# Kernel tuning notes

Hardware: AMD Instinct MI355X
Metric: run time of the kernel (lower is better)

The kernel has to match this reference:

```python
import jax, jax.numpy as jnp
import numpy as np
from jax import lax

B, L, D_MODEL = 2, 2048, 768
D_STATE, D_INNER, DT_RANK, K = 16, 1536, 48, 4


def setup_inputs() -> dict:
    key = jax.random.key(0)
    ks = jax.random.split(key, 10)
    x = jax.random.normal(ks[0], (B, L, D_MODEL), dtype=jnp.float32)
    in_proj_w = 0.02 * jax.random.normal(ks[1], (2 * D_INNER, D_MODEL), dtype=jnp.float32)
    conv_w = 0.1 * jax.random.normal(ks[2], (D_INNER, 1, K), dtype=jnp.float32)
    conv_b = 0.01 * jax.random.normal(ks[3], (D_INNER,), dtype=jnp.float32)
    # A_log initialized as log(1..d_state) per channel (as in _init_parameters)
    A_log = jnp.tile(jnp.log(jnp.arange(1, D_STATE + 1, dtype=jnp.float32)), (D_INNER, 1))
    D_param = jnp.ones((D_INNER,), dtype=jnp.float32)
    x_proj_w = 0.02 * jax.random.normal(ks[4], (DT_RANK + 2 * D_STATE, D_INNER), dtype=jnp.float32)
    dt_proj_w = jax.random.uniform(ks[5], (D_INNER, DT_RANK), minval=-0.1, maxval=0.1, dtype=jnp.float32)
    dt_proj_b = 0.01 * jax.random.normal(ks[6], (D_INNER,), dtype=jnp.float32)
    out_proj_w = 0.02 * jax.random.normal(ks[7], (D_MODEL, D_INNER), dtype=jnp.float32)
    return {"x": x, "in_proj_w": in_proj_w, "conv_w": conv_w, "conv_b": conv_b,
            "A_log": A_log, "D_param": D_param, "x_proj_w": x_proj_w,
            "dt_proj_w": dt_proj_w, "dt_proj_b": dt_proj_b, "out_proj_w": out_proj_w}


def _forward(x, in_proj_w, conv_w, conv_b, A_log, D_param, x_proj_w, dt_proj_w, dt_proj_b, out_proj_w):
    xz = jnp.einsum('bld,ed->ble', x, in_proj_w)            # [B,L,2*d_inner]
    xp, z = jnp.split(xz, 2, axis=-1)                        # [B,L,d_inner] each
    # depthwise causal conv1d: torch Conv1d(padding=3)[..., :L] == left-pad 3, valid conv
    xc = lax.conv_general_dilated(
        xp.transpose(0, 2, 1), conv_w, window_strides=(1,),
        padding=[(K - 1, 0)], feature_group_count=D_INNER)   # [B,d_inner,L]
    xc = (xc + conv_b[None, :, None]).transpose(0, 2, 1)     # [B,L,d_inner]
    xc = jax.nn.silu(xc)
    x_dbl = jnp.einsum('bld,ed->ble', xc, x_proj_w)          # [B,L,dt_rank+2*d_state]
    dt_low, Bmat, Cmat = jnp.split(x_dbl, [DT_RANK, DT_RANK + D_STATE], axis=-1)
    dt = jax.nn.softplus(jnp.einsum('blr,dr->bld', dt_low, dt_proj_w) + dt_proj_b)  # [B,L,d_inner]
    A = -jnp.exp(A_log)                                      # [d_inner,d_state]
    A_bar = jnp.exp(dt[..., None] * A[None, None])           # [B,L,d_inner,d_state]
    Bx = (dt * xc)[..., None] * Bmat[:, :, None, :]          # [B,L,d_inner,d_state]
    # time-major scan over the recurrence h = A_bar*h + B_bar*x
    A_t = A_bar.transpose(1, 0, 2, 3)
    Bx_t = Bx.transpose(1, 0, 2, 3)
    C_t = Cmat.transpose(1, 0, 2)                            # [L,B,d_state]
    h0 = jnp.zeros((B, D_INNER, D_STATE), dtype=x.dtype)

    def step(h, inp):
        a, bx, c = inp
        h = a * h + bx
        y = jnp.einsum('bds,bs->bd', h, c)
        return h, y

    _, ys = lax.scan(step, h0, (A_t, Bx_t, C_t))             # ys: [L,B,d_inner]
    y = ys.transpose(1, 0, 2)
    y = y + xc * D_param
    y = y * jax.nn.silu(z)
    return jnp.einsum('bld,md->blm', y, out_proj_w)          # [B,L,d_model]


def reference(x, in_proj_w, conv_w, conv_b, A_log, D_param, x_proj_w, dt_proj_w, dt_proj_b, out_proj_w):
    return _forward(x, in_proj_w, conv_w, conv_b, A_log, D_param, x_proj_w, dt_proj_w, dt_proj_b, out_proj_w)
```

## Files before the change

kernel.cpp:

```cpp
#include <hip/hip_runtime.h>
#include <stdint.h>

#define B_SZ    2
#define L_SEQ   2048
#define DMODEL  768
#define DSTATE  16
#define DINNER  1536
#define DTRANK  48
#define M_ROWS  4096
#define NSEG    8
#define SEGL    256
#define NSC     8
#define SCL     32
#define KSPLIT  8

typedef __attribute__((ext_vector_type(8))) short bf16x8;
typedef __attribute__((ext_vector_type(4))) float f32x4;
typedef __attribute__((ext_vector_type(2))) float f32x2;
typedef __attribute__((ext_vector_type(4))) unsigned int u32x4;
typedef __attribute__((ext_vector_type(2))) unsigned int u32x2;

__device__ __forceinline__ unsigned short f2bf(float f) {
  unsigned int u = __float_as_uint(f);
  u += 0x7FFFu + ((u >> 16) & 1u);
  return (unsigned short)(u >> 16);
}
__device__ __forceinline__ unsigned int pack2bf(float a, float b) {
  return (unsigned int)f2bf(a) | ((unsigned int)f2bf(b) << 16);
}
__device__ __forceinline__ float bf2f(unsigned short h) {
  return __uint_as_float(((unsigned int)h) << 16);
}
__device__ __forceinline__ float fexp(float x) {
  return __builtin_amdgcn_exp2f(x * 1.44269504088896340736f);
}
__device__ __forceinline__ float sigm(float x) {
  return 1.0f / (1.0f + fexp(-x));
}

template <int CTRL>
__device__ __forceinline__ float dpp_add(float v) {
  int x = __builtin_amdgcn_update_dpp(0, __float_as_int(v), CTRL, 0xF, 0xF, true);
  return v + __int_as_float(x);
}
__device__ __forceinline__ float quad_sum(float v) {
  v = dpp_add<0xB1>(v);
  v = dpp_add<0x4E>(v);
  return v;
}
__device__ __forceinline__ float row16_sum(float v) {
  v = dpp_add<0xB1>(v);
  v = dpp_add<0x4E>(v);
  v = dpp_add<0x124>(v);
  v = dpp_add<0x128>(v);
  return v;
}

__global__ void cast_all_kernel(const float* __restrict__ x, const float* __restrict__ w1,
                                const float* __restrict__ w2, const float* __restrict__ w3,
                                const float* __restrict__ dtw,
                                unsigned short* __restrict__ xbf, unsigned short* __restrict__ w1bf,
                                unsigned short* __restrict__ w2bf, unsigned short* __restrict__ w3bf,
                                unsigned short* __restrict__ dtwbf) {
  int i = blockIdx.x * 256 + threadIdx.x;
  const int n_x = M_ROWS * DMODEL;
  const int n_w1 = 2 * DINNER * DMODEL;
  const int n_w3 = DMODEL * DINNER;
  const int n_w2 = 128 * DINNER;
  const int n_dtw = DINNER * 64;
  if (i < n_x)  { xbf[i] = f2bf(x[i]); return; }  i -= n_x;
  if (i < n_w1) { w1bf[i] = f2bf(w1[i]); return; } i -= n_w1;
  if (i < n_w3) { w3bf[i] = f2bf(w3[i]); return; } i -= n_w3;
  if (i < n_w2) {
    int row = i / DINNER, col = i - row * DINNER;
    w2bf[i] = (row < (DTRANK + 2 * DSTATE)) ? f2bf(w2[row * DINNER + col]) : (unsigned short)0;
    return;
  }
  i -= n_w2;
  if (i < n_dtw) {
    int row = i >> 6, col = i & 63;
    dtwbf[i] = (col < DTRANK) ? f2bf(dtw[row * DTRANK + col]) : (unsigned short)0;
  }
}

__global__ void xdbl_pack_kernel(const float* __restrict__ xdblS,
                                 unsigned short* __restrict__ dtlbf,
                                 float* __restrict__ BCt) {
  const int SLAB = M_ROWS * 128;
  int i = blockIdx.x * 256 + threadIdx.x;
  const int n_dtl = M_ROWS * 64;
  if (i < n_dtl) {
    int row = i >> 6, col = i & 63;
    if (col < DTRANK) {
      float v = 0.f;
#pragma unroll
      for (int z = 0; z < KSPLIT; z++) v += xdblS[(size_t)z * SLAB + row * 128 + col];
      dtlbf[i] = f2bf(v);
    } else dtlbf[i] = 0;
    return;
  }
  i -= n_dtl;
  int l4 = i & 511;
  int j  = (i >> 9) & 31;
  int b  = (i >> 14) & 1;
  f32x4 o;
#pragma unroll
  for (int k = 0; k < 4; k++) {
    float v = 0.f;
    size_t base = ((size_t)b * L_SEQ + l4 * 4 + k) * 128 + DTRANK + j;
#pragma unroll
    for (int z = 0; z < KSPLIT; z++) v += xdblS[(size_t)z * SLAB + base];
    o[k] = v;
  }
  *(f32x4*)(BCt + ((size_t)b * 32 + j) * L_SEQ + l4 * 4) = o;
}

template <int EPI>
__global__ __launch_bounds__(256, 2) void gemm_bt(
    const unsigned short* __restrict__ A, const unsigned short* __restrict__ Bt,
    float* __restrict__ C, int K, int KS, int ldc, long slab,
    const float* __restrict__ bias) {
  __shared__ unsigned short As[128 * 40];
  __shared__ unsigned short Bs[128 * 40];
  const int tid = threadIdx.x;
  const int m0 = blockIdx.x * 128;
  const int n0 = blockIdx.y * 128;
  const int ks = blockIdx.z * KS, ke = ks + KS;
  float* Cz = C + (size_t)blockIdx.z * slab;
  const int lane = tid & 63;
  const int wave = tid >> 6;
  const int wr = (wave >> 1) * 64, wc = (wave & 1) * 64;
  const int lm = lane & 15, q = lane >> 4;
  const int r = tid >> 2, sg = (tid & 3) * 8;

  f32x4 acc[4][4] = {};

  for (int k0 = ks; k0 < ke; k0 += 32) {
    u32x4 a0 = *(const u32x4*)(A + (size_t)(m0 + r) * K + k0 + sg);
    u32x4 a1 = *(const u32x4*)(A + (size_t)(m0 + r + 64) * K + k0 + sg);
    u32x4 b0 = *(const u32x4*)(Bt + (size_t)(n0 + r) * K + k0 + sg);
    u32x4 b1 = *(const u32x4*)(Bt + (size_t)(n0 + r + 64) * K + k0 + sg);
    __syncthreads();
    *(u32x4*)&As[r * 40 + sg] = a0;
    *(u32x4*)&As[(r + 64) * 40 + sg] = a1;
    *(u32x4*)&Bs[r * 40 + sg] = b0;
    *(u32x4*)&Bs[(r + 64) * 40 + sg] = b1;
    __syncthreads();
    bf16x8 af[4], bq[4];
#pragma unroll
    for (int mt = 0; mt < 4; mt++)
      af[mt] = *(const bf16x8*)&As[(wr + mt * 16 + lm) * 40 + q * 8];
#pragma unroll
    for (int nt = 0; nt < 4; nt++)
      bq[nt] = *(const bf16x8*)&Bs[(wc + nt * 16 + lm) * 40 + q * 8];
#pragma unroll
    for (int mt = 0; mt < 4; mt++)
#pragma unroll
      for (int nt = 0; nt < 4; nt++)
        acc[mt][nt] = __builtin_amdgcn_mfma_f32_16x16x32_bf16(af[mt], bq[nt], acc[mt][nt], 0, 0, 0);
  }

#pragma unroll
  for (int mt = 0; mt < 4; mt++) {
    int row0 = m0 + wr + mt * 16 + q * 4;
    float bs4[4];
    if (EPI == 2) {
#pragma unroll
      for (int i = 0; i < 4; i++) bs4[i] = bias[row0 + i];
    }
#pragma unroll
    for (int nt = 0; nt < 4; nt++) {
      int col = n0 + wc + nt * 16 + lm;
#pragma unroll
      for (int i = 0; i < 4; i++) {
        float v = acc[mt][nt][i];
        if (EPI == 2) {
          v += bs4[i];
          v = (v > 15.f) ? v : log1pf(fexp(v));
        }
        Cz[(size_t)(row0 + i) * ldc + col] = v;
      }
    }
  }
}

__global__ __launch_bounds__(256) void conv_silu_t(const float* __restrict__ xz,
                                                   const float* __restrict__ cw,
                                                   const float* __restrict__ cb,
                                                   unsigned short* __restrict__ xcbf,
                                                   unsigned short* __restrict__ xcT) {
  __shared__ float tl[67 * 68];
  __shared__ unsigned short xs[64 * 80];
  __shared__ float cws[64 * 4];
  __shared__ float cbs[64];
  const int r0 = blockIdx.x * 64;
  const int c0 = blockIdx.y * 64;
  const int t = threadIdx.x;
  cws[t] = cw[(c0 + (t >> 2)) * 4 + (t & 3)];
  if (t < 64) cbs[t] = cb[c0 + t];
  const bool lowedge = (r0 & (L_SEQ - 1)) == 0;
#pragma unroll
  for (int it = 0; it < 5; it++) {
    int idx = t + it * 256;
    int rr = idx >> 4;
    int cs4 = (idx & 15) * 4;
    if (rr < 67) {
      f32x4 v;
      if (lowedge && rr < 3) v = (f32x4){0.f, 0.f, 0.f, 0.f};
      else v = *(const f32x4*)(xz + (size_t)(r0 + rr - 3) * 3072 + c0 + cs4);
      *(f32x4*)&tl[rr * 68 + cs4] = v;
    }
  }
  __syncthreads();
  const int cs = (t & 15) * 4;
  f32x4 w0, w1, w2, w3, cbv;
#pragma unroll
  for (int j = 0; j < 4; j++) {
    w0[j] = cws[(cs + j) * 4 + 0];
    w1[j] = cws[(cs + j) * 4 + 1];
    w2[j] = cws[(cs + j) * 4 + 2];
    w3[j] = cws[(cs + j) * 4 + 3];
    cbv[j] = cbs[cs + j];
  }
#pragma unroll
  for (int it = 0; it < 4; it++) {
    int r = (t >> 4) + it * 16;
    f32x4 t0 = *(const f32x4*)&tl[(r + 0) * 68 + cs];
    f32x4 t1 = *(const f32x4*)&tl[(r + 1) * 68 + cs];
    f32x4 t2 = *(const f32x4*)&tl[(r + 2) * 68 + cs];
    f32x4 t3 = *(const f32x4*)&tl[(r + 3) * 68 + cs];
    f32x4 acc = cbv + w0 * t0 + w1 * t1 + w2 * t2 + w3 * t3;
#pragma unroll
    for (int j = 0; j < 4; j++) acc[j] = acc[j] * sigm(acc[j]);
    u32x2 pk;
    pk[0] = pack2bf(acc[0], acc[1]);
    pk[1] = pack2bf(acc[2], acc[3]);
    *(u32x2*)(xcbf + (size_t)(r0 + r) * DINNER + c0 + cs) = pk;
    *(u32x2*)&xs[r * 80 + cs] = pk;
  }
  __syncthreads();
#pragma unroll
  for (int it = 0; it < 2; it++) {
    int idx = t + it * 256;
    int cc = idx & 63, rs = idx >> 6;
    unsigned int w[4];
#pragma unroll
    for (int p = 0; p < 4; p++) {
      unsigned int lo = xs[(rs * 8 + 2 * p) * 80 + cc];
      unsigned int hi = xs[(rs * 8 + 2 * p + 1) * 80 + cc];
      w[p] = lo | (hi << 16);
    }
    *(u32x4*)(xcT + (size_t)(c0 + cc) * M_ROWS + r0 + rs * 8) = *(u32x4*)w;
  }
}

__global__ __launch_bounds__(256) void transpose_silu(const float* __restrict__ xz,
                                                      unsigned short* __restrict__ out) {
  __shared__ float tl[64 * 68];
  const int r0 = blockIdx.x * 64;
  const int c0 = blockIdx.y * 64;
  const int tid = threadIdx.x;
#pragma unroll
  for (int it = 0; it < 4; it++) {
    int idx = tid + it * 256;
    int rr = idx >> 4, cs = idx & 15;
    f32x4 v = *(const f32x4*)(xz + (size_t)(r0 + rr) * 3072 + DINNER + c0 + cs * 4);
#pragma unroll
    for (int p = 0; p < 4; p++) v[p] = v[p] * sigm(v[p]);
    *(f32x4*)&tl[rr * 68 + cs * 4] = v;
  }
  __syncthreads();
#pragma unroll
  for (int it = 0; it < 2; it++) {
    int idx = tid + it * 256;
    int cc = idx & 63, rs = idx >> 6;
    unsigned int w[4];
#pragma unroll
    for (int p = 0; p < 4; p++)
      w[p] = pack2bf(tl[(rs * 8 + 2 * p) * 68 + cc], tl[(rs * 8 + 2 * p + 1) * 68 + cc]);
    *(u32x4*)(out + (size_t)(c0 + cc) * M_ROWS + r0 + rs * 8) = *(u32x4*)w;
  }
}

struct SC32 { f32x2 dt; unsigned int xc, sz; f32x4 B0, B1, C0, C1; };

template <int FULL>
__global__ __launch_bounds__(64) void scan_seg(
    const float* __restrict__ dtT, const unsigned short* __restrict__ xcT,
    const float* __restrict__ BCt, const unsigned short* __restrict__ szT,
    const float* __restrict__ A_log, const float* __restrict__ Dp,
    const float* __restrict__ HIN, float* __restrict__ P, float* __restrict__ HL,
    unsigned short* __restrict__ ybf) {
  __shared__ float dtS[4 * 36];
  __shared__ float dtxS[4 * 36];
  __shared__ float BS[16 * 36];
  __shared__ float CS[FULL ? 16 * 36 : 1];
  __shared__ unsigned int xcR[FULL ? 4 * 18 : 1];
  __shared__ unsigned int szR[FULL ? 4 * 18 : 1];
  __shared__ float ysh[FULL ? 16 * 36 : 1];
  const int lane = threadIdx.x;
  const int s = lane & 15, dl = lane >> 4;
  const int d0 = blockIdx.x * 4;
  const int d = d0 + dl;
  const int b = blockIdx.y;
  const int seg = blockIdx.z;
  const int lseg = seg * SEGL;
  const size_t rbase = (size_t)b * L_SEQ + lseg;
  const float a2 = -fexp(A_log[d * 16 + s]) * 1.44269504f;
  const float dpv = Dp[d];
  const float* dtbase = dtT + (size_t)d0 * M_ROWS + rbase;
  const unsigned short* xcbase = xcT + (size_t)d0 * M_ROWS + rbase;
  const unsigned short* szbase = szT + (size_t)d0 * M_ROWS + rbase;
  const float* Bbase = BCt + (size_t)b * 32 * L_SEQ + lseg;
  const float* Cbase = Bbase + 16 * L_SEQ;
  const int ch = lane >> 4, li = lane & 15;
  const int s4 = lane >> 2, lj = lane & 3;
  float* ywp = &ysh[(dl * 4 + (s >> 2)) * 36 + (s & 3)];
  const bool sb0 = (s & 1) != 0, sb1 = (s & 2) != 0;
  float h = 0.f, sdt = 0.f;
  size_t o = (((size_t)seg * B_SZ + b) * DINNER + d) * 16 + s;
  if (FULL) h = HIN[o];

  auto load32 = [&](SC32& R, int l0) {
    R.dt = *(const f32x2*)(dtbase + (size_t)ch * M_ROWS + l0 + li * 2);
    R.xc = *(const unsigned int*)(xcbase + (size_t)ch * M_ROWS + l0 + li * 2);
    if (FULL) R.sz = *(const unsigned int*)(szbase + (size_t)ch * M_ROWS + l0 + li * 2);
    R.B0 = *(const f32x4*)(Bbase + (size_t)s4 * L_SEQ + l0 + lj * 8);
    R.B1 = *(const f32x4*)(Bbase + (size_t)s4 * L_SEQ + l0 + lj * 8 + 4);
    if (FULL) {
      R.C0 = *(const f32x4*)(Cbase + (size_t)s4 * L_SEQ + l0 + lj * 8);
      R.C1 = *(const f32x4*)(Cbase + (size_t)s4 * L_SEQ + l0 + lj * 8 + 4);
    }
  };
  auto store32 = [&](const SC32& R) {
    if (!FULL) sdt += R.dt[0] + R.dt[1];
    f32x2 xf, dtx;
    xf[0] = __uint_as_float(R.xc << 16);
    xf[1] = __uint_as_float(R.xc & 0xFFFF0000u);
    dtx = R.dt * xf;
    *(f32x2*)&dtS[ch * 36 + li * 2] = R.dt;
    *(f32x2*)&dtxS[ch * 36 + li * 2] = dtx;
    if (FULL) {
      xcR[ch * 18 + li] = R.xc;
      szR[ch * 18 + li] = R.sz;
    }
    *(f32x4*)&BS[s4 * 36 + lj * 8] = R.B0;
    *(f32x4*)&BS[s4 * 36 + lj * 8 + 4] = R.B1;
    if (FULL) {
      *(f32x4*)&CS[s4 * 36 + lj * 8] = R.C0;
      *(f32x4*)&CS[s4 * 36 + lj * 8 + 4] = R.C1;
    }
  };

#pragma unroll 1
  for (int c = 0; c < NSC; c++) {
    SC32 R;
    load32(R, c * SCL);
    store32(R);
#pragma unroll
    for (int g = 0; g < 4; g++) {
      const int l0g = g * 8;
      f32x4 dta = *(const f32x4*)&dtS[dl * 36 + l0g];
      f32x4 dtb = *(const f32x4*)&dtS[dl * 36 + l0g + 4];
      f32x4 xa  = *(const f32x4*)&dtxS[dl * 36 + l0g];
      f32x4 xb  = *(const f32x4*)&dtxS[dl * 36 + l0g + 4];
      f32x4 Ba  = *(const f32x4*)&BS[s * 36 + l0g];
      f32x4 Bb  = *(const f32x4*)&BS[s * 36 + l0g + 4];
      f32x4 Ca, Cb;
      if (FULL) {
        Ca = *(const f32x4*)&CS[s * 36 + l0g];
        Cb = *(const f32x4*)&CS[s * 36 + l0g + 4];
      }
      float p8[8];
#pragma unroll
      for (int j = 0; j < 8; j++) {
        float dtj = (j < 4) ? dta[j] : dtb[j - 4];
        float dxj = (j < 4) ? xa[j]  : xb[j - 4];
        float Bj  = (j < 4) ? Ba[j]  : Bb[j - 4];
        float a = __builtin_amdgcn_exp2f(dtj * a2);
        h = a * h + dxj * Bj;
        if (FULL) {
          float Cj = (j < 4) ? Ca[j] : Cb[j - 4];
          p8[j] = h * Cj;
        }
      }
      if (FULL) {
#pragma unroll
        for (int half = 0; half < 2; half++) {
          float q0 = quad_sum(p8[half * 4 + 0]);
          float q1 = quad_sum(p8[half * 4 + 1]);
          float q2 = quad_sum(p8[half * 4 + 2]);
          float q3 = quad_sum(p8[half * 4 + 3]);
          float v01 = sb0 ? q1 : q0;
          float v23 = sb0 ? q3 : q2;
          ywp[g * 8 + half * 4] = sb1 ? v23 : v01;
        }
      }
    }
    if (FULL) {
      f32x2 y0 = *(const f32x2*)&ysh[(dl * 4 + 0) * 36 + s * 2];
      f32x2 y1 = *(const f32x2*)&ysh[(dl * 4 + 1) * 36 + s * 2];
      f32x2 y2 = *(const f32x2*)&ysh[(dl * 4 + 2) * 36 + s * 2];
      f32x2 y3 = *(const f32x2*)&ysh[(dl * 4 + 3) * 36 + s * 2];
      f32x2 ys = y0 + y1 + y2 + y3;
      unsigned int xcu = xcR[dl * 18 + s];
      unsigned int szu = szR[dl * 18 + s];
      float xcf[2] = {__uint_as_float(xcu << 16), __uint_as_float(xcu & 0xFFFF0000u)};
      float szf[2] = {__uint_as_float(szu << 16), __uint_as_float(szu & 0xFFFF0000u)};
      size_t rr0 = rbase + c * SCL + s * 2;
#pragma unroll
      for (int i = 0; i < 2; i++) {
        float yv = ys[i] + xcf[i] * dpv;
        ybf[(rr0 + i) * DINNER + d] = f2bf(yv * szf[i]);
      }
    }
  }
  if (!FULL) {
    sdt = row16_sum(sdt);
    P[o] = __builtin_amdgcn_exp2f(a2 * sdt);
    HL[o] = h;
  }
}

__global__ void scan_comb(const float* __restrict__ P, const float* __restrict__ HL,
                          float* __restrict__ HIN) {
  int tg = blockIdx.x * 256 + threadIdx.x;
  int s = tg & 15;
  int rem = tg >> 4;
  int d = rem % DINNER;
  int b = rem / DINNER;
  float h = 0.f;
  for (int g = 0; g < NSEG; g++) {
    size_t o = (((size_t)g * B_SZ + b) * DINNER + d) * 16 + s;
    HIN[o] = h;
    if (g < NSEG - 1) h = P[o] * h + HL[o];
  }
}

extern "C" void kernel_launch(void* const* d_in, const int* in_sizes, int n_in,
                              void* d_out, int out_size, void* d_ws, size_t ws_size,
                              hipStream_t stream) {
  const float* x    = (const float*)d_in[0];
  const float* w1   = (const float*)d_in[1];
  const float* cw   = (const float*)d_in[2];
  const float* cb   = (const float*)d_in[3];
  const float* alog = (const float*)d_in[4];
  const float* Dp   = (const float*)d_in[5];
  const float* w2   = (const float*)d_in[6];
  const float* dtw  = (const float*)d_in[7];
  const float* dtb  = (const float*)d_in[8];
  const float* w3   = (const float*)d_in[9];
  float* out = (float*)d_out;
  char* ws = (char*)d_ws;

  size_t off = 0;
  auto alloc = [&](size_t bytes) { size_t o = off; off += (bytes + 255) & ~(size_t)255; return o; };
  char*           xzr   = ws + alloc((size_t)M_ROWS * 3072 * 4);
  float*          xz    = (float*)xzr;
  float*          dtT   = (float*)xzr;
  unsigned short* ybf   = (unsigned short*)(xzr + (size_t)DINNER * M_ROWS * 4);
  float*          xdblS = (float*)(ws + alloc((size_t)KSPLIT * M_ROWS * 128 * 4));
  unsigned short* xbf   = (unsigned short*)(ws + alloc((size_t)M_ROWS * DMODEL * 2));
  unsigned short* w1bf  = (unsigned short*)(ws + alloc((size_t)2 * DINNER * DMODEL * 2));
  unsigned short* w2bf  = (unsigned short*)(ws + alloc((size_t)128 * DINNER * 2));
  unsigned short* w3bf  = (unsigned short*)(ws + alloc((size_t)DMODEL * DINNER * 2));
  unsigned short* dtlbf = (unsigned short*)(ws + alloc((size_t)M_ROWS * 64 * 2));
  unsigned short* dtwbf = (unsigned short*)(ws + alloc((size_t)DINNER * 64 * 2));
  unsigned short* xcbf  = (unsigned short*)(ws + alloc((size_t)M_ROWS * DINNER * 2));
  unsigned short* xcT   = (unsigned short*)(ws + alloc((size_t)DINNER * M_ROWS * 2));
  unsigned short* szbf  = (unsigned short*)(ws + alloc((size_t)DINNER * M_ROWS * 2));
  float*          BCt   = (float*)(ws + alloc((size_t)B_SZ * 32 * L_SEQ * 4));
  float*          Pbuf  = (float*)(ws + alloc((size_t)NSEG * B_SZ * DINNER * 16 * 4));
  float*          HLbuf = (float*)(ws + alloc((size_t)NSEG * B_SZ * DINNER * 16 * 4));
  float*          HINb  = (float*)(ws + alloc((size_t)NSEG * B_SZ * DINNER * 16 * 4));

  cast_all_kernel<<<27264, 256, 0, stream>>>(x, w1, w2, w3, dtw, xbf, w1bf, w2bf, w3bf, dtwbf);
  gemm_bt<0><<<dim3(32, 24), 256, 0, stream>>>(xbf, w1bf, xz, DMODEL, DMODEL, 3072, 0, nullptr);
  conv_silu_t<<<dim3(64, 24), 256, 0, stream>>>(xz, cw, cb, xcbf, xcT);
  transpose_silu<<<dim3(64, 24), 256, 0, stream>>>(xz, szbf);
  gemm_bt<0><<<dim3(32, 1, KSPLIT), 256, 0, stream>>>(xcbf, w2bf, xdblS, DINNER,
                                                      DINNER / KSPLIT, 128,
                                                      (long)M_ROWS * 128, nullptr);
  xdbl_pack_kernel<<<1152, 256, 0, stream>>>(xdblS, dtlbf, BCt);
  gemm_bt<2><<<dim3(12, 32), 256, 0, stream>>>(dtwbf, dtlbf, dtT, 64, 64, M_ROWS, 0, dtb);
  scan_seg<0><<<dim3(384, 2, NSEG - 1), 64, 0, stream>>>(dtT, xcT, BCt, szbf, alog, Dp,
                                                         nullptr, Pbuf, HLbuf, nullptr);
  scan_comb<<<192, 256, 0, stream>>>(Pbuf, HLbuf, HINb);
  scan_seg<1><<<dim3(384, 2, NSEG), 64, 0, stream>>>(dtT, xcT, BCt, szbf, alog, Dp,
                                                     HINb, nullptr, nullptr, ybf);
  gemm_bt<0><<<dim3(32, 6), 256, 0, stream>>>(ybf, w3bf, out, DINNER, DINNER, 768, 0, nullptr);
}
```

Measured before the change: 304.6 us.

## Use direct global-to-LDS loads in GEMMs, fuse z-transpose into conv, widen scan blocks

The three plain GEMMs now use a new kernel that moves tiles straight from global memory into LDS through global_load_lds. This drops the register staging step, but the LDS tile loses its padding, which risks bank conflicts. The separate silu(z) transpose kernel is merged into the conv kernel to save one launch and reuse the tile buffer. The scan kernels now pack four independent waves into each 256-thread block instead of one wave per block.

```diff
diff --git a/kernel.cpp b/kernel.cpp
--- a/kernel.cpp
+++ b/kernel.cpp
@@ -28,9 +28,6 @@
 __device__ __forceinline__ unsigned int pack2bf(float a, float b) {
   return (unsigned int)f2bf(a) | ((unsigned int)f2bf(b) << 16);
 }
-__device__ __forceinline__ float bf2f(unsigned short h) {
-  return __uint_as_float(((unsigned int)h) << 16);
-}
 __device__ __forceinline__ float fexp(float x) {
   return __builtin_amdgcn_exp2f(x * 1.44269504088896340736f);
 }
@@ -54,6 +51,11 @@
   v = dpp_add<0x124>(v);
   v = dpp_add<0x128>(v);
   return v;
+}
+
+__device__ __forceinline__ void gload_lds(const unsigned short* g, unsigned short* l) {
+  __builtin_amdgcn_global_load_lds((__attribute__((address_space(1))) void*)g,
+                                   (__attribute__((address_space(3))) void*)l, 16, 0, 0);
 }
 
 __global__ void cast_all_kernel(const float* __restrict__ x, const float* __restrict__ w1,
@@ -115,18 +117,68 @@
   *(f32x4*)(BCt + ((size_t)b * 32 + j) * L_SEQ + l4 * 4) = o;
 }
 
-template <int EPI>
-__global__ __launch_bounds__(256, 2) void gemm_bt(
+__global__ __launch_bounds__(256, 2) void gemm_async(
     const unsigned short* __restrict__ A, const unsigned short* __restrict__ Bt,
-    float* __restrict__ C, int K, int KS, int ldc, long slab,
-    const float* __restrict__ bias) {
+    float* __restrict__ C, int K, int KS, int ldc, long slab) {
+  __shared__ unsigned short As[128 * 32];
+  __shared__ unsigned short Bs[128 * 32];
+  const int tid = threadIdx.x;
+  const int lane = tid & 63;
+  const int wv = tid >> 6;
+  const int m0 = blockIdx.x * 128;
+  const int n0 = blockIdx.y * 128;
+  const int ks = blockIdx.z * KS, ke = ks + KS;
+  float* Cz = C + (size_t)blockIdx.z * slab;
+  const int wr = (wv >> 1) * 64, wc = (wv & 1) * 64;
+  const int lm = lane & 15, q = lane >> 4;
+  const int srow = wv * 16 + (lane >> 2);
+  const int scol = (lane & 3) * 8;
+
+  f32x4 acc[4][4] = {};
+
+  for (int k0 = ks; k0 < ke; k0 += 32) {
+#pragma unroll
+    for (int j = 0; j < 2; j++) {
+      gload_lds(A + (size_t)(m0 + j * 64 + srow) * K + k0 + scol, &As[(j * 64 + wv * 16) * 32]);
+      gload_lds(Bt + (size_t)(n0 + j * 64 + srow) * K + k0 + scol, &Bs[(j * 64 + wv * 16) * 32]);
+    }
+    __syncthreads();
+    bf16x8 af[4], bq[4];
+#pragma unroll
+    for (int mt = 0; mt < 4; mt++)
+      af[mt] = *(const bf16x8*)&As[(wr + mt * 16 + lm) * 32 + q * 8];
+#pragma unroll
+    for (int nt = 0; nt < 4; nt++)
+      bq[nt] = *(const bf16x8*)&Bs[(wc + nt * 16 + lm) * 32 + q * 8];
+#pragma unroll
+    for (int mt = 0; mt < 4; mt++)
+#pragma unroll
+      for (int nt = 0; nt < 4; nt++)
+        acc[mt][nt] = __builtin_amdgcn_mfma_f32_16x16x32_bf16(af[mt], bq[nt], acc[mt][nt], 0, 0, 0);
+    __syncthreads();
+  }
+
+#pragma unroll
+  for (int mt = 0; mt < 4; mt++) {
+    int row0 = m0 + wr + mt * 16 + q * 4;
+#pragma unroll
+    for (int nt = 0; nt < 4; nt++) {
+      int col = n0 + wc + nt * 16 + lm;
+#pragma unroll
+      for (int i = 0; i < 4; i++)
+        Cz[(size_t)(row0 + i) * ldc + col] = acc[mt][nt][i];
+    }
+  }
+}
+
+__global__ __launch_bounds__(256, 2) void gemm_dt(
+    const unsigned short* __restrict__ A, const unsigned short* __restrict__ Bt,
+    float* __restrict__ C, int K, int ldc, const float* __restrict__ bias) {
   __shared__ unsigned short As[128 * 40];
   __shared__ unsigned short Bs[128 * 40];
   const int tid = threadIdx.x;
   const int m0 = blockIdx.x * 128;
   const int n0 = blockIdx.y * 128;
-  const int ks = blockIdx.z * KS, ke = ks + KS;
-  float* Cz = C + (size_t)blockIdx.z * slab;
   const int lane = tid & 63;
   const int wave = tid >> 6;
   const int wr = (wave >> 1) * 64, wc = (wave & 1) * 64;
@@ -135,7 +187,7 @@
 
   f32x4 acc[4][4] = {};
 
-  for (int k0 = ks; k0 < ke; k0 += 32) {
+  for (int k0 = 0; k0 < K; k0 += 32) {
     u32x4 a0 = *(const u32x4*)(A + (size_t)(m0 + r) * K + k0 + sg);
     u32x4 a1 = *(const u32x4*)(A + (size_t)(m0 + r + 64) * K + k0 + sg);
     u32x4 b0 = *(const u32x4*)(Bt + (size_t)(n0 + r) * K + k0 + sg);
@@ -164,34 +216,30 @@
   for (int mt = 0; mt < 4; mt++) {
     int row0 = m0 + wr + mt * 16 + q * 4;
     float bs4[4];
-    if (EPI == 2) {
-#pragma unroll
-      for (int i = 0; i < 4; i++) bs4[i] = bias[row0 + i];
-    }
+#pragma unroll
+    for (int i = 0; i < 4; i++) bs4[i] = bias[row0 + i];
 #pragma unroll
     for (int nt = 0; nt < 4; nt++) {
       int col = n0 + wc + nt * 16 + lm;
 #pragma unroll
       for (int i = 0; i < 4; i++) {
-        float v = acc[mt][nt][i];
-        if (EPI == 2) {
-          v += bs4[i];
-          v = (v > 15.f) ? v : log1pf(fexp(v));
-        }
-        Cz[(size_t)(row0 + i) * ldc + col] = v;
+        float v = acc[mt][nt][i] + bs4[i];
+        v = (v > 15.f) ? v : log1pf(fexp(v));
+        C[(size_t)(row0 + i) * ldc + col] = v;
       }
     }
   }
 }
 
-__global__ __launch_bounds__(256) void conv_silu_t(const float* __restrict__ xz,
-                                                   const float* __restrict__ cw,
-                                                   const float* __restrict__ cb,
-                                                   unsigned short* __restrict__ xcbf,
-                                                   unsigned short* __restrict__ xcT) {
+__global__ __launch_bounds__(256) void conv_silu_zt(const float* __restrict__ xz,
+                                                    const float* __restrict__ cw,
+                                                    const float* __restrict__ cb,
+                                                    unsigned short* __restrict__ xcbf,
+                                                    unsigned short* __restrict__ xcT,
+                                                    unsigned short* __restrict__ szT) {
   __shared__ float tl[67 * 68];
   __shared__ unsigned short xs[64 * 80];
-  __shared__ float cws[64 * 4];
+  __shared__ float cws[256];
   __shared__ float cbs[64];
   const int r0 = blockIdx.x * 64;
   const int c0 = blockIdx.y * 64;
@@ -212,33 +260,44 @@
     }
   }
   __syncthreads();
-  const int cs = (t & 15) * 4;
-  f32x4 w0, w1, w2, w3, cbv;
-#pragma unroll
-  for (int j = 0; j < 4; j++) {
-    w0[j] = cws[(cs + j) * 4 + 0];
-    w1[j] = cws[(cs + j) * 4 + 1];
-    w2[j] = cws[(cs + j) * 4 + 2];
-    w3[j] = cws[(cs + j) * 4 + 3];
-    cbv[j] = cbs[cs + j];
-  }
+  {
+    const int cs = (t & 15) * 4;
+    f32x4 w0, w1, w2, w3, cbv;
+#pragma unroll
+    for (int j = 0; j < 4; j++) {
+      w0[j] = cws[(cs + j) * 4 + 0];
+      w1[j] = cws[(cs + j) * 4 + 1];
+      w2[j] = cws[(cs + j) * 4 + 2];
+      w3[j] = cws[(cs + j) * 4 + 3];
+      cbv[j] = cbs[cs + j];
+    }
+#pragma unroll
+    for (int it = 0; it < 4; it++) {
+      int r = (t >> 4) + it * 16;
+      f32x4 t0 = *(const f32x4*)&tl[(r + 0) * 68 + cs];
+      f32x4 t1 = *(const f32x4*)&tl[(r + 1) * 68 + cs];
+      f32x4 t2 = *(const f32x4*)&tl[(r + 2) * 68 + cs];
+      f32x4 t3 = *(const f32x4*)&tl[(r + 3) * 68 + cs];
+      f32x4 acc = cbv + w0 * t0 + w1 * t1 + w2 * t2 + w3 * t3;
+#pragma unroll
+      for (int j = 0; j < 4; j++) acc[j] = acc[j] * sigm(acc[j]);
+      u32x2 pk;
+      pk[0] = pack2bf(acc[0], acc[1]);
+      pk[1] = pack2bf(acc[2], acc[3]);
+      *(u32x2*)(xcbf + (size_t)(r0 + r) * DINNER + c0 + cs) = pk;
+      *(u32x2*)&xs[r * 80 + cs] = pk;
+    }
+  }
+  __syncthreads();
 #pragma unroll
   for (int it = 0; it < 4; it++) {
-    int r = (t >> 4) + it * 16;
-    f32x4 t0 = *(const f32x4*)&tl[(r + 0) * 68 + cs];
-    f32x4 t1 = *(const f32x4*)&tl[(r + 1) * 68 + cs];
-    f32x4 t2 = *(const f32x4*)&tl[(r + 2) * 68 + cs];
-    f32x4 t3 = *(const f32x4*)&tl[(r + 3) * 68 + cs];
-    f32x4 acc = cbv + w0 * t0 + w1 * t1 + w2 * t2 + w3 * t3;
-#pragma unroll
-    for (int j = 0; j < 4; j++) acc[j] = acc[j] * sigm(acc[j]);
-    u32x2 pk;
-    pk[0] = pack2bf(acc[0], acc[1]);
-    pk[1] = pack2bf(acc[2], acc[3]);
-    *(u32x2*)(xcbf + (size_t)(r0 + r) * DINNER + c0 + cs) = pk;
-    *(u32x2*)&xs[r * 80 + cs] = pk;
-  }
-  __syncthreads();
+    int idx = t + it * 256;
+    int rr = idx >> 4, cs = idx & 15;
+    f32x4 v = *(const f32x4*)(xz + (size_t)(r0 + rr) * 3072 + DINNER + c0 + cs * 4);
+#pragma unroll
+    for (int p = 0; p < 4; p++) v[p] = v[p] * sigm(v[p]);
+    *(f32x4*)&tl[rr * 68 + cs * 4] = v;
+  }
 #pragma unroll
   for (int it = 0; it < 2; it++) {
     int idx = t + it * 256;
@@ -252,55 +311,40 @@
     }
     *(u32x4*)(xcT + (size_t)(c0 + cc) * M_ROWS + r0 + rs * 8) = *(u32x4*)w;
   }
-}
-
-__global__ __launch_bounds__(256) void transpose_silu(const float* __restrict__ xz,
-                                                      unsigned short* __restrict__ out) {
-  __shared__ float tl[64 * 68];
-  const int r0 = blockIdx.x * 64;
-  const int c0 = blockIdx.y * 64;
-  const int tid = threadIdx.x;
-#pragma unroll
-  for (int it = 0; it < 4; it++) {
-    int idx = tid + it * 256;
-    int rr = idx >> 4, cs = idx & 15;
-    f32x4 v = *(const f32x4*)(xz + (size_t)(r0 + rr) * 3072 + DINNER + c0 + cs * 4);
-#pragma unroll
-    for (int p = 0; p < 4; p++) v[p] = v[p] * sigm(v[p]);
-    *(f32x4*)&tl[rr * 68 + cs * 4] = v;
-  }
   __syncthreads();
 #pragma unroll
   for (int it = 0; it < 2; it++) {
-    int idx = tid + it * 256;
+    int idx = t + it * 256;
     int cc = idx & 63, rs = idx >> 6;
     unsigned int w[4];
 #pragma unroll
     for (int p = 0; p < 4; p++)
       w[p] = pack2bf(tl[(rs * 8 + 2 * p) * 68 + cc], tl[(rs * 8 + 2 * p + 1) * 68 + cc]);
-    *(u32x4*)(out + (size_t)(c0 + cc) * M_ROWS + r0 + rs * 8) = *(u32x4*)w;
+    *(u32x4*)(szT + (size_t)(c0 + cc) * M_ROWS + r0 + rs * 8) = *(u32x4*)w;
   }
 }
 
 struct SC32 { f32x2 dt; unsigned int xc, sz; f32x4 B0, B1, C0, C1; };
 
 template <int FULL>
-__global__ __launch_bounds__(64) void scan_seg(
+__global__ __launch_bounds__(256) void scan_seg(
     const float* __restrict__ dtT, const unsigned short* __restrict__ xcT,
     const float* __restrict__ BCt, const unsigned short* __restrict__ szT,
     const float* __restrict__ A_log, const float* __restrict__ Dp,
     const float* __restrict__ HIN, float* __restrict__ P, float* __restrict__ HL,
     unsigned short* __restrict__ ybf) {
-  __shared__ float dtS[4 * 36];
-  __shared__ float dtxS[4 * 36];
-  __shared__ float BS[16 * 36];
-  __shared__ float CS[FULL ? 16 * 36 : 1];
-  __shared__ unsigned int xcR[FULL ? 4 * 18 : 1];
-  __shared__ unsigned int szR[FULL ? 4 * 18 : 1];
-  __shared__ float ysh[FULL ? 16 * 36 : 1];
-  const int lane = threadIdx.x;
+  __shared__ float dtS[4][4 * 36];
+  __shared__ float dtxS[4][4 * 36];
+  __shared__ float BS[4][16 * 36];
+  __shared__ float CS[FULL ? 4 : 1][FULL ? 16 * 36 : 1];
+  __shared__ unsigned int xcR[FULL ? 4 : 1][FULL ? 4 * 18 : 1];
+  __shared__ unsigned int szR[FULL ? 4 : 1][FULL ? 4 * 18 : 1];
+  __shared__ float ysh[FULL ? 4 : 1][FULL ? 16 * 36 : 1];
+  const int tid = threadIdx.x;
+  const int wv = tid >> 6;
+  const int lane = tid & 63;
   const int s = lane & 15, dl = lane >> 4;
-  const int d0 = blockIdx.x * 4;
+  const int d0 = blockIdx.x * 16 + wv * 4;
   const int d = d0 + dl;
   const int b = blockIdx.y;
   const int seg = blockIdx.z;
@@ -315,7 +359,11 @@
   const float* Cbase = Bbase + 16 * L_SEQ;
   const int ch = lane >> 4, li = lane & 15;
   const int s4 = lane >> 2, lj = lane & 3;
-  float* ywp = &ysh[(dl * 4 + (s >> 2)) * 36 + (s & 3)];
+  float* dtSw = dtS[wv];
+  float* dtxSw = dtxS[wv];
+  float* BSw = BS[wv];
+  float* CSw = FULL ? CS[wv] : nullptr;
+  float* ywp = FULL ? &ysh[wv][(dl * 4 + (s >> 2)) * 36 + (s & 3)] : nullptr;
   const bool sb0 = (s & 1) != 0, sb1 = (s & 2) != 0;
   float h = 0.f, sdt = 0.f;
   size_t o = (((size_t)seg * B_SZ + b) * DINNER + d) * 16 + s;
@@ -338,17 +386,17 @@
     xf[0] = __uint_as_float(R.xc << 16);
     xf[1] = __uint_as_float(R.xc & 0xFFFF0000u);
     dtx = R.dt * xf;
-    *(f32x2*)&dtS[ch * 36 + li * 2] = R.dt;
-    *(f32x2*)&dtxS[ch * 36 + li * 2] = dtx;
+    *(f32x2*)&dtSw[ch * 36 + li * 2] = R.dt;
+    *(f32x2*)&dtxSw[ch * 36 + li * 2] = dtx;
     if (FULL) {
-      xcR[ch * 18 + li] = R.xc;
-      szR[ch * 18 + li] = R.sz;
-    }
-    *(f32x4*)&BS[s4 * 36 + lj * 8] = R.B0;
-    *(f32x4*)&BS[s4 * 36 + lj * 8 + 4] = R.B1;
+      xcR[wv][ch * 18 + li] = R.xc;
+      szR[wv][ch * 18 + li] = R.sz;
+    }
+    *(f32x4*)&BSw[s4 * 36 + lj * 8] = R.B0;
+    *(f32x4*)&BSw[s4 * 36 + lj * 8 + 4] = R.B1;
     if (FULL) {
-      *(f32x4*)&CS[s4 * 36 + lj * 8] = R.C0;
-      *(f32x4*)&CS[s4 * 36 + lj * 8 + 4] = R.C1;
+      *(f32x4*)&CSw[s4 * 36 + lj * 8] = R.C0;
+      *(f32x4*)&CSw[s4 * 36 + lj * 8 + 4] = R.C1;
     }
   };
 
@@ -360,16 +408,16 @@
 #pragma unroll
     for (int g = 0; g < 4; g++) {
       const int l0g = g * 8;
-      f32x4 dta = *(const f32x4*)&dtS[dl * 36 + l0g];
-      f32x4 dtb = *(const f32x4*)&dtS[dl * 36 + l0g + 4];
-      f32x4 xa  = *(const f32x4*)&dtxS[dl * 36 + l0g];
-      f32x4 xb  = *(const f32x4*)&dtxS[dl * 36 + l0g + 4];
-      f32x4 Ba  = *(const f32x4*)&BS[s * 36 + l0g];
-      f32x4 Bb  = *(const f32x4*)&BS[s * 36 + l0g + 4];
+      f32x4 dta = *(const f32x4*)&dtSw[dl * 36 + l0g];
+      f32x4 dtb = *(const f32x4*)&dtSw[dl * 36 + l0g + 4];
+      f32x4 xa  = *(const f32x4*)&dtxSw[dl * 36 + l0g];
+      f32x4 xb  = *(const f32x4*)&dtxSw[dl * 36 + l0g + 4];
+      f32x4 Ba  = *(const f32x4*)&BSw[s * 36 + l0g];
+      f32x4 Bb  = *(const f32x4*)&BSw[s * 36 + l0g + 4];
       f32x4 Ca, Cb;
       if (FULL) {
-        Ca = *(const f32x4*)&CS[s * 36 + l0g];
-        Cb = *(const f32x4*)&CS[s * 36 + l0g + 4];
+        Ca = *(const f32x4*)&CSw[s * 36 + l0g];
+        Cb = *(const f32x4*)&CSw[s * 36 + l0g + 4];
       }
       float p8[8];
 #pragma unroll
@@ -398,13 +446,13 @@
       }
     }
     if (FULL) {
-      f32x2 y0 = *(const f32x2*)&ysh[(dl * 4 + 0) * 36 + s * 2];
-      f32x2 y1 = *(const f32x2*)&ysh[(dl * 4 + 1) * 36 + s * 2];
-      f32x2 y2 = *(const f32x2*)&ysh[(dl * 4 + 2) * 36 + s * 2];
-      f32x2 y3 = *(const f32x2*)&ysh[(dl * 4 + 3) * 36 + s * 2];
+      f32x2 y0 = *(const f32x2*)&ysh[wv][(dl * 4 + 0) * 36 + s * 2];
+      f32x2 y1 = *(const f32x2*)&ysh[wv][(dl * 4 + 1) * 36 + s * 2];
+      f32x2 y2 = *(const f32x2*)&ysh[wv][(dl * 4 + 2) * 36 + s * 2];
+      f32x2 y3 = *(const f32x2*)&ysh[wv][(dl * 4 + 3) * 36 + s * 2];
       f32x2 ys = y0 + y1 + y2 + y3;
-      unsigned int xcu = xcR[dl * 18 + s];
-      unsigned int szu = szR[dl * 18 + s];
+      unsigned int xcu = xcR[wv][dl * 18 + s];
+      unsigned int szu = szR[wv][dl * 18 + s];
       float xcf[2] = {__uint_as_float(xcu << 16), __uint_as_float(xcu & 0xFFFF0000u)};
       float szf[2] = {__uint_as_float(szu << 16), __uint_as_float(szu & 0xFFFF0000u)};
       size_t rr0 = rbase + c * SCL + s * 2;
@@ -475,18 +523,17 @@
   float*          HINb  = (float*)(ws + alloc((size_t)NSEG * B_SZ * DINNER * 16 * 4));
 
   cast_all_kernel<<<27264, 256, 0, stream>>>(x, w1, w2, w3, dtw, xbf, w1bf, w2bf, w3bf, dtwbf);
-  gemm_bt<0><<<dim3(32, 24), 256, 0, stream>>>(xbf, w1bf, xz, DMODEL, DMODEL, 3072, 0, nullptr);
-  conv_silu_t<<<dim3(64, 24), 256, 0, stream>>>(xz, cw, cb, xcbf, xcT);
-  transpose_silu<<<dim3(64, 24), 256, 0, stream>>>(xz, szbf);
-  gemm_bt<0><<<dim3(32, 1, KSPLIT), 256, 0, stream>>>(xcbf, w2bf, xdblS, DINNER,
+  gemm_async<<<dim3(32, 24), 256, 0, stream>>>(xbf, w1bf, xz, DMODEL, DMODEL, 3072, 0);
+  conv_silu_zt<<<dim3(64, 24), 256, 0, stream>>>(xz, cw, cb, xcbf, xcT, szbf);
+  gemm_async<<<dim3(32, 1, KSPLIT), 256, 0, stream>>>(xcbf, w2bf, xdblS, DINNER,
                                                       DINNER / KSPLIT, 128,
-                                                      (long)M_ROWS * 128, nullptr);
+                                                      (long)M_ROWS * 128);
   xdbl_pack_kernel<<<1152, 256, 0, stream>>>(xdblS, dtlbf, BCt);
-  gemm_bt<2><<<dim3(12, 32), 256, 0, stream>>>(dtwbf, dtlbf, dtT, 64, 64, M_ROWS, 0, dtb);
-  scan_seg<0><<<dim3(384, 2, NSEG - 1), 64, 0, stream>>>(dtT, xcT, BCt, szbf, alog, Dp,
+  gemm_dt<<<dim3(12, 32), 256, 0, stream>>>(dtwbf, dtlbf, dtT, 64, M_ROWS, dtb);
+  scan_seg<0><<<dim3(96, 2, NSEG - 1), 256, 0, stream>>>(dtT, xcT, BCt, szbf, alog, Dp,
                                                          nullptr, Pbuf, HLbuf, nullptr);
   scan_comb<<<192, 256, 0, stream>>>(Pbuf, HLbuf, HINb);
-  scan_seg<1><<<dim3(384, 2, NSEG), 64, 0, stream>>>(dtT, xcT, BCt, szbf, alog, Dp,
+  scan_seg<1><<<dim3(96, 2, NSEG), 256, 0, stream>>>(dtT, xcT, BCt, szbf, alog, Dp,
                                                      HINb, nullptr, nullptr, ybf);
-  gemm_bt<0><<<dim3(32, 6), 256, 0, stream>>>(ybf, w3bf, out, DINNER, DINNER, 768, 0, nullptr);
-}
+  gemm_async<<<dim3(32, 6), 256, 0, stream>>>(ybf, w3bf, out, DINNER, DINNER, 768, 0);
+}
```

Result: faster. 295.2 us (-3.1%).
